# Performance work log

Hardware: AMD Instinct MI355X
Metric: run time of the kernel (lower is better)

Reference implementation:

```python
import jax, jax.numpy as jnp
import numpy as np

B, S, D, H = 2, 2048, 1024, 16
DK = D // H


def setup_inputs() -> dict:
    key = jax.random.key(0)
    ks = jax.random.split(key, 10)
    scale = 1.0 / np.sqrt(D)
    x = jax.random.normal(ks[0], (B, S, D), dtype=jnp.float32)
    # causal mask: 1 = attend, 0 = masked (module's create_causal_mask)
    mask = jnp.tril(jnp.ones((S, S), dtype=jnp.int32))[None, None]
    Wq = jax.random.normal(ks[1], (D, D), jnp.float32) * scale
    bq = jax.random.normal(ks[2], (D,), jnp.float32) * 0.01
    Wk = jax.random.normal(ks[3], (D, D), jnp.float32) * scale
    bk = jax.random.normal(ks[4], (D,), jnp.float32) * 0.01
    Wv = jax.random.normal(ks[5], (D, D), jnp.float32) * scale
    bv = jax.random.normal(ks[6], (D,), jnp.float32) * 0.01
    Wo = jax.random.normal(ks[7], (D, D), jnp.float32) * scale
    bo = jax.random.normal(ks[8], (D,), jnp.float32) * 0.01
    return {"x": x, "mask": mask, "Wq": Wq, "bq": bq, "Wk": Wk, "bk": bk,
            "Wv": Wv, "bv": bv, "Wo": Wo, "bo": bo}


def reference(x, mask, Wq, bq, Wk, bk, Wv, bv, Wo, bo):
    b, s, _ = x.shape
    # projections; [B,S,D] -> [B,H,S,DK]
    def split_heads(t):
        return t.reshape(b, s, H, DK).transpose(0, 2, 1, 3)
    Q = split_heads(x @ Wq + bq)
    K = split_heads(x @ Wk + bk)
    V = split_heads(x @ Wv + bv)
    scores = jnp.einsum('bhqd,bhkd->bhqk', Q, K) / np.sqrt(DK)
    scores = jnp.where(mask == 0, jnp.float32(-1e9), scores)
    attn = jax.nn.softmax(scores, axis=-1)  # dropout p=0 -> identity
    ctx = jnp.einsum('bhqk,bhkd->bhqd', attn, V)
    ctx = ctx.transpose(0, 2, 1, 3).reshape(b, s, D)
    return ctx @ Wo + bo
```

## Files before the change

### kernel.cpp

```cpp
#include <hip/hip_runtime.h>
#include <hip/hip_bf16.h>


typedef _Float16 f16x8 __attribute__((ext_vector_type(8)));
typedef _Float16 f16x4 __attribute__((ext_vector_type(4)));
typedef _Float16 f16x2 __attribute__((ext_vector_type(2)));
typedef float f32x4 __attribute__((ext_vector_type(4)));

#define QSCALE 0.180336880111112f

__device__ __forceinline__ void async_copy16(const _Float16* gsrc,
                                             _Float16* ldst) {
  __builtin_amdgcn_global_load_lds(
      (const __attribute__((address_space(1))) void*)gsrc,
      (__attribute__((address_space(3))) void*)ldst, 16, 0, 0);
}

__global__ __launch_bounds__(256) void prep(
    const float* __restrict__ x, _Float16* __restrict__ xh,
    const float* __restrict__ W0, const float* __restrict__ W1,
    const float* __restrict__ W2, const float* __restrict__ W3,
    _Float16* __restrict__ T0, _Float16* __restrict__ T1,
    _Float16* __restrict__ T2, _Float16* __restrict__ T3) {
  if (blockIdx.x < 4096) {
    int i = (blockIdx.x * 256 + threadIdx.x) * 4;
    float4 v = *(const float4*)(x + i);
    f16x4 o;
    o.x = (_Float16)v.x; o.y = (_Float16)v.y;
    o.z = (_Float16)v.z; o.w = (_Float16)v.w;
    *(f16x4*)(xh + i) = o;
    return;
  }
  const int id = blockIdx.x - 4096;
  const int w = id >> 10, rem = id & 1023;
  const int bx = rem & 31, by = rem >> 5;
  const float* W; _Float16* T;
  switch (w) {
    case 0: W = W0; T = T0; break;
    case 1: W = W1; T = T1; break;
    case 2: W = W2; T = T2; break;
    default: W = W3; T = T3; break;
  }
  __shared__ _Float16 tile[32][33];
  const int tx = threadIdx.x & 31, ty = threadIdx.x >> 5;
  const int n0 = bx * 32, k0 = by * 32;
  for (int i = 0; i < 4; i++) {
    int kk = k0 + ty + i * 8;
    tile[ty + i * 8][tx] = (_Float16)W[(size_t)kk * 1024 + n0 + tx];
  }
  __syncthreads();
  for (int i = 0; i < 4; i++) {
    int nn = n0 + ty + i * 8;
    T[(size_t)nn * 1024 + k0 + tx] = tile[tx][ty + i * 8];
  }
}

__global__ __launch_bounds__(256) void gemm_qkv(
    const _Float16* __restrict__ A, const _Float16* __restrict__ BtAll,
    const float* __restrict__ bq, const float* __restrict__ bk,
    const float* __restrict__ bv, _Float16* __restrict__ Qh,
    _Float16* __restrict__ Kh, _Float16* __restrict__ VT) {
  __shared__ _Float16 As[128 * 32];
  __shared__ _Float16 Bs[128 * 32];
  const int tid = threadIdx.x;
  const int wave = tid >> 6, lane = tid & 63;
  const int lr = lane & 15, lq = lane >> 4;
  const int m0 = blockIdx.x * 128, n0 = blockIdx.y * 128;
  const int rw = (wave & 1) * 64, cw = (wave >> 1) * 64;

  const int sel = blockIdx.y >> 3;
  const float* bias = sel == 0 ? bq : (sel == 1 ? bk : bv);
  const int c0 = n0 & 1023;

  f32x4 acc[4][4] = {};
  const int r0 = wave * 32 + (lane >> 2);
  const int woff = (lane & 3) * 8;

  for (int kt = 0; kt < 1024; kt += 32) {
    __syncthreads();
    async_copy16(A + (size_t)(m0 + r0) * 1024 + kt + woff, As + r0 * 32 + woff);
    async_copy16(A + (size_t)(m0 + r0 + 16) * 1024 + kt + woff,
                 As + (r0 + 16) * 32 + woff);
    async_copy16(BtAll + (size_t)(n0 + r0) * 1024 + kt + woff,
                 Bs + r0 * 32 + woff);
    async_copy16(BtAll + (size_t)(n0 + r0 + 16) * 1024 + kt + woff,
                 Bs + (r0 + 16) * 32 + woff);
    __syncthreads();
    f16x8 af[4], bf[4];
    for (int i = 0; i < 4; i++)
      af[i] = *(const f16x8*)(As + (rw + i * 16 + lr) * 32 + lq * 8);
    for (int j = 0; j < 4; j++)
      bf[j] = *(const f16x8*)(Bs + (cw + j * 16 + lr) * 32 + lq * 8);
    for (int i = 0; i < 4; i++)
      for (int j = 0; j < 4; j++)
        acc[i][j] = __builtin_amdgcn_mfma_f32_16x16x32_f16(af[i], bf[j],
                                                           acc[i][j], 0, 0, 0);
  }

  if (sel == 2) {
    for (int i = 0; i < 4; i++) {
      const int row = m0 + rw + i * 16 + lq * 4;
      const int bb = row >> 11, ss = row & 2047;
      for (int j = 0; j < 4; j++) {
        const int col = c0 + cw + j * 16 + lr;
        const int hh = col >> 6, dk = col & 63;
        const float bvl = bias[col];
        f16x4 pv;
        for (int r = 0; r < 4; r++) pv[r] = (_Float16)(acc[i][j][r] + bvl);
        *(f16x4*)(VT + ((size_t)(bb * 16 + hh) * 64 + dk) * 2048 + ss) = pv;
      }
    }
  } else {
    _Float16* out = sel == 0 ? Qh : Kh;
    const float scl = sel == 0 ? QSCALE : 1.0f;
    for (int i = 0; i < 4; i++) {
      const int row = m0 + rw + i * 16 + lq * 4;
      for (int j = 0; j < 4; j++) {
        const int col = c0 + cw + j * 16 + lr;
        const float bvl = bias[col];
        for (int r = 0; r < 4; r++)
          out[(size_t)(row + r) * 1024 + col] =
              (_Float16)((acc[i][j][r] + bvl) * scl);
      }
    }
  }
}

__global__ __launch_bounds__(256) void gemm_out(
    const _Float16* __restrict__ A, const _Float16* __restrict__ Bt,
    const float* __restrict__ bias, float* __restrict__ out) {
  __shared__ _Float16 As[128 * 32];
  __shared__ _Float16 Bs[64 * 32];
  const int tid = threadIdx.x;
  const int wave = tid >> 6, lane = tid & 63;
  const int lr = lane & 15, lq = lane >> 4;
  const int m0 = blockIdx.x * 128, n0 = blockIdx.y * 64;
  const int rw = (wave & 1) * 64, cw = (wave >> 1) * 32;
  f32x4 acc[4][2] = {};
  const int r0 = wave * 32 + (lane >> 2);
  const int br = tid >> 2;
  const int woff = (lane & 3) * 8;

  for (int kt = 0; kt < 1024; kt += 32) {
    __syncthreads();
    async_copy16(A + (size_t)(m0 + r0) * 1024 + kt + woff, As + r0 * 32 + woff);
    async_copy16(A + (size_t)(m0 + r0 + 16) * 1024 + kt + woff,
                 As + (r0 + 16) * 32 + woff);
    async_copy16(Bt + (size_t)(n0 + br) * 1024 + kt + woff,
                 Bs + br * 32 + woff);
    __syncthreads();
    f16x8 af[4], bf[2];
    for (int i = 0; i < 4; i++)
      af[i] = *(const f16x8*)(As + (rw + i * 16 + lr) * 32 + lq * 8);
    for (int j = 0; j < 2; j++)
      bf[j] = *(const f16x8*)(Bs + (cw + j * 16 + lr) * 32 + lq * 8);
    for (int i = 0; i < 4; i++)
      for (int j = 0; j < 2; j++)
        acc[i][j] = __builtin_amdgcn_mfma_f32_16x16x32_f16(af[i], bf[j],
                                                           acc[i][j], 0, 0, 0);
  }
  for (int i = 0; i < 4; i++) {
    const int row = m0 + rw + i * 16 + lq * 4;
    for (int j = 0; j < 2; j++) {
      const int col = n0 + cw + j * 16 + lr;
      const float bvl = bias[col];
      for (int r = 0; r < 4; r++)
        out[(size_t)(row + r) * 1024 + col] = acc[i][j][r] + bvl;
    }
  }
}

__global__ __launch_bounds__(256) void attn(const _Float16* __restrict__ Q,
                                            const _Float16* __restrict__ K,
                                            const _Float16* __restrict__ VT,
                                            _Float16* __restrict__ ctx) {
  const int qt = 15 - blockIdx.y;
  const int bh = blockIdx.x;
  const int b = bh >> 4, h = bh & 15;
  const int tid = threadIdx.x, wave = tid >> 6, lane = tid & 63;
  const int lr = lane & 15, lq = lane >> 4;
  const int qmin = qt * 128 + wave * 32;
  const size_t qkbase = ((size_t)b * 2048) * 1024 + h * 64;
  const size_t vtbase = ((size_t)bh) * 64 * 2048;

  __shared__ _Float16 Ks[2][64 * 72];
  __shared__ _Float16 Vs[2][64 * 72];

  f16x8 qf[2][2];
  for (int m = 0; m < 2; m++) {
    const _Float16* qp =
        Q + qkbase + (size_t)(qmin + m * 16 + lr) * 1024 + lq * 8;
    qf[m][0] = *(const f16x8*)qp;
    qf[m][1] = *(const f16x8*)(qp + 32);
  }

  float mrow[2] = {-1e30f, -1e30f}, lsum[2] = {0.f, 0.f};
  f32x4 o[2][4] = {};

  const int sgr = tid >> 2, sgc = (tid & 3) * 8;
  const _Float16* Kg0 = K + qkbase + (size_t)sgr * 1024 + sgc;
  const _Float16* Vg0 = VT + vtbase + (size_t)sgr * 2048 + sgc;
  uint4 ka = *(const uint4*)Kg0, kb = *(const uint4*)(Kg0 + 32);
  uint4 va = *(const uint4*)Vg0, vb = *(const uint4*)(Vg0 + 32);

  const int tmax = 2 * qt + 1;
  for (int t = 0;; t++) {
    _Float16* ksb = Ks[t & 1];
    _Float16* vsb = Vs[t & 1];
    *(uint4*)(ksb + sgr * 72 + sgc) = ka;
    *(uint4*)(ksb + sgr * 72 + sgc + 32) = kb;
    *(uint4*)(vsb + sgr * 72 + sgc) = va;
    *(uint4*)(vsb + sgr * 72 + sgc + 32) = vb;
    __syncthreads();
    if (t < tmax) {
      const _Float16* kg = Kg0 + (size_t)(t + 1) * 64 * 1024;
      const _Float16* vg = Vg0 + (t + 1) * 64;
      ka = *(const uint4*)kg; kb = *(const uint4*)(kg + 32);
      va = *(const uint4*)vg; vb = *(const uint4*)(vg + 32);
    }

    const int kv0 = t * 64;
    f32x4 s[2][4];
    for (int ks = 0; ks < 4; ks++) {
      f16x8 k0 = *(const f16x8*)(ksb + (ks * 16 + lr) * 72 + lq * 8);
      f16x8 k1 = *(const f16x8*)(ksb + (ks * 16 + lr) * 72 + 32 + lq * 8);
      for (int m = 0; m < 2; m++) {
        f32x4 z = {};
        z = __builtin_amdgcn_mfma_f32_16x16x32_f16(k0, qf[m][0], z, 0, 0, 0);
        z = __builtin_amdgcn_mfma_f32_16x16x32_f16(k1, qf[m][1], z, 0, 0, 0);
        s[m][ks] = z;
      }
    }
    if (kv0 + 63 > qmin) {
      for (int m = 0; m < 2; m++) {
        const int qcol = qmin + m * 16 + lr;
        for (int ks = 0; ks < 4; ks++)
          for (int r = 0; r < 4; r++)
            if (kv0 + ks * 16 + lq * 4 + r > qcol) s[m][ks][r] = -1e30f;
      }
    }
    f16x4 pa[2][4];
    float alpha[2];
    for (int m = 0; m < 2; m++) {
      float mx = s[m][0][0];
      for (int ks = 0; ks < 4; ks++)
        for (int r = 0; r < 4; r++) mx = fmaxf(mx, s[m][ks][r]);
      mx = fmaxf(mx, __shfl_xor(mx, 16));
      mx = fmaxf(mx, __shfl_xor(mx, 32));
      float mnew = fmaxf(mrow[m], mx);
      alpha[m] = exp2f(mrow[m] - mnew);
      mrow[m] = mnew;
      float rs = 0.f;
      for (int ks = 0; ks < 4; ks++) {
        float p0 = exp2f(s[m][ks][0] - mnew);
        float p1 = exp2f(s[m][ks][1] - mnew);
        float p2 = exp2f(s[m][ks][2] - mnew);
        float p3 = exp2f(s[m][ks][3] - mnew);
        rs += (p0 + p1) + (p2 + p3);
        f16x2 q01 =
            __builtin_bit_cast(f16x2, __builtin_amdgcn_cvt_pkrtz(p0, p1));
        f16x2 q23 =
            __builtin_bit_cast(f16x2, __builtin_amdgcn_cvt_pkrtz(p2, p3));
        pa[m][ks] = __builtin_shufflevector(q01, q23, 0, 1, 2, 3);
      }
      rs += __shfl_xor(rs, 16);
      rs += __shfl_xor(rs, 32);
      lsum[m] = lsum[m] * alpha[m] + rs;
    }
    if (__any((alpha[0] != 1.0f) | (alpha[1] != 1.0f))) {
      for (int m = 0; m < 2; m++) {
        float ar[4];
        for (int r = 0; r < 4; r++) ar[r] = __shfl(alpha[m], lq * 4 + r);
        for (int dn = 0; dn < 4; dn++)
          for (int r = 0; r < 4; r++) o[m][dn][r] *= ar[r];
      }
    }
    for (int ks = 0; ks < 4; ks++)
      for (int dn = 0; dn < 4; dn++) {
        f16x4 vf =
            *(const f16x4*)(vsb + (dn * 16 + lr) * 72 + ks * 16 + lq * 4);
        for (int m = 0; m < 2; m++)
          o[m][dn] = __builtin_amdgcn_mfma_f32_16x16x16f16(pa[m][ks], vf,
                                                           o[m][dn], 0, 0, 0);
      }
    if (t == tmax) break;
  }

  for (int m = 0; m < 2; m++) {
    for (int r = 0; r < 4; r++) {
      float lv = __shfl(lsum[m], lq * 4 + r);
      float inv = 1.0f / lv;
      const int row = qmin + m * 16 + lq * 4 + r;
      for (int dn = 0; dn < 4; dn++)
        ctx[qkbase + (size_t)row * 1024 + dn * 16 + lr] =
            (_Float16)(o[m][dn][r] * inv);
    }
  }
}

extern "C" void kernel_launch(void* const* d_in, const int* in_sizes, int n_in,
                              void* d_out, int out_size, void* d_ws,
                              size_t ws_size, hipStream_t stream) {
  const float* x  = (const float*)d_in[0];
  const float* Wq = (const float*)d_in[2];
  const float* bq = (const float*)d_in[3];
  const float* Wk = (const float*)d_in[4];
  const float* bk = (const float*)d_in[5];
  const float* Wv = (const float*)d_in[6];
  const float* bv = (const float*)d_in[7];
  const float* Wo = (const float*)d_in[8];
  const float* bo = (const float*)d_in[9];
  float* out = (float*)d_out;

  char* ws = (char*)d_ws;
  const size_t MB = 1 << 20;
  _Float16* xh  = (_Float16*)(ws);
  _Float16* WTs = (_Float16*)(ws + 8 * MB);
  _Float16* WqT = WTs;
  _Float16* WkT = (_Float16*)(ws + 10 * MB);
  _Float16* WvT = (_Float16*)(ws + 12 * MB);
  _Float16* WoT = (_Float16*)(ws + 14 * MB);
  _Float16* Qh  = (_Float16*)(ws + 16 * MB);
  _Float16* Kh  = (_Float16*)(ws + 24 * MB);
  _Float16* VT  = (_Float16*)(ws + 32 * MB);
  _Float16* ctx = (_Float16*)(ws);

  prep<<<8192, 256, 0, stream>>>(x, xh, Wq, Wk, Wv, Wo, WqT, WkT, WvT, WoT);
  gemm_qkv<<<dim3(32, 24), 256, 0, stream>>>(xh, WTs, bq, bk, bv, Qh, Kh, VT);
  attn<<<dim3(32, 16), 256, 0, stream>>>(Qh, Kh, VT, ctx);
  gemm_out<<<dim3(32, 16), 256, 0, stream>>>(ctx, WoT, bo, out);
}
```

Baseline: 215.4 us.

## Shrink attention tiles, balance causal work, MFMA row sums, coalesce V transpose

The attention kernel now uses 64-query blocks with 128 threads and a 32-row grid, with a snake-ordered query-tile mapping meant to even out causal work across blocks. The diagonal mask is applied only on the last tile. The softmax row sum is now computed with an extra MFMA against a ones vector instead of shuffle reductions, and a trailing barrier protects the double buffer. The V-transpose epilogue of the QKV GEMM is staged through shared memory so global stores become coalesced 16-byte writes, at the cost of extra LDS use and barriers.

```diff
diff --git a/kernel.cpp b/kernel.cpp
--- a/kernel.cpp
+++ b/kernel.cpp
@@ -62,6 +62,7 @@
     _Float16* __restrict__ Kh, _Float16* __restrict__ VT) {
   __shared__ _Float16 As[128 * 32];
   __shared__ _Float16 Bs[128 * 32];
+  __shared__ _Float16 tbuf[64 * 136];
   const int tid = threadIdx.x;
   const int wave = tid >> 6, lane = tid & 63;
   const int lr = lane & 15, lq = lane >> 4;
@@ -98,16 +99,29 @@
   }
 
   if (sel == 2) {
-    for (int i = 0; i < 4; i++) {
-      const int row = m0 + rw + i * 16 + lq * 4;
-      const int bb = row >> 11, ss = row & 2047;
-      for (int j = 0; j < 4; j++) {
-        const int col = c0 + cw + j * 16 + lr;
-        const int hh = col >> 6, dk = col & 63;
-        const float bvl = bias[col];
-        f16x4 pv;
-        for (int r = 0; r < 4; r++) pv[r] = (_Float16)(acc[i][j][r] + bvl);
-        *(f16x4*)(VT + ((size_t)(bb * 16 + hh) * 64 + dk) * 2048 + ss) = pv;
+    const int bb = m0 >> 11, ss0 = m0 & 2047;
+    const int cs = tid & 15, dkr = tid >> 4;
+    for (int jj = 0; jj < 2; jj++) {
+      __syncthreads();
+      if ((wave >> 1) == jj) {
+        for (int i = 0; i < 4; i++) {
+          const int sl = rw + i * 16 + lq * 4;
+          for (int j = 0; j < 4; j++) {
+            const int dk = j * 16 + lr;
+            const float bvl = bias[c0 + jj * 64 + dk];
+            f16x4 pv;
+            for (int r = 0; r < 4; r++) pv[r] = (_Float16)(acc[i][j][r] + bvl);
+            *(f16x4*)(tbuf + dk * 136 + sl) = pv;
+          }
+        }
+      }
+      __syncthreads();
+      const int hh = (c0 + jj * 64) >> 6;
+      _Float16* dst = VT + ((size_t)(bb * 16 + hh) * 64) * 2048 + ss0;
+      for (int k = 0; k < 4; k++) {
+        const int dk = dkr + k * 16;
+        *(uint4*)(dst + (size_t)dk * 2048 + cs * 8) =
+            *(const uint4*)(tbuf + dk * 136 + cs * 8);
       }
     }
   } else {
@@ -170,16 +184,23 @@
   }
 }
 
-__global__ __launch_bounds__(256) void attn(const _Float16* __restrict__ Q,
+__global__ __launch_bounds__(128) void attn(const _Float16* __restrict__ Q,
                                             const _Float16* __restrict__ K,
                                             const _Float16* __restrict__ VT,
                                             _Float16* __restrict__ ctx) {
-  const int qt = 15 - blockIdx.y;
+  const int qy = blockIdx.y, li = qy & 7;
+  int qt;
+  switch (qy >> 3) {
+    case 0: qt = 31 - li; break;
+    case 1: qt = 16 + li; break;
+    case 2: qt = 15 - li; break;
+    default: qt = li; break;
+  }
   const int bh = blockIdx.x;
   const int b = bh >> 4, h = bh & 15;
   const int tid = threadIdx.x, wave = tid >> 6, lane = tid & 63;
   const int lr = lane & 15, lq = lane >> 4;
-  const int qmin = qt * 128 + wave * 32;
+  const int qmin = qt * 64 + wave * 32;
   const size_t qkbase = ((size_t)b * 2048) * 1024 + h * 64;
   const size_t vtbase = ((size_t)bh) * 64 * 2048;
 
@@ -193,33 +214,42 @@
     qf[m][0] = *(const f16x8*)qp;
     qf[m][1] = *(const f16x8*)(qp + 32);
   }
-
-  float mrow[2] = {-1e30f, -1e30f}, lsum[2] = {0.f, 0.f};
+  f16x4 onesf;
+  {
+    _Float16 ov = (lr == 0) ? (_Float16)1.0f : (_Float16)0.0f;
+    for (int i = 0; i < 4; i++) onesf[i] = ov;
+  }
+
+  float mrow[2] = {-1e30f, -1e30f};
   f32x4 o[2][4] = {};
-
-  const int sgr = tid >> 2, sgc = (tid & 3) * 8;
+  f32x4 ol[2] = {};
+
+  const int sgr = tid >> 1, sgc = (tid & 1) * 32;
   const _Float16* Kg0 = K + qkbase + (size_t)sgr * 1024 + sgc;
   const _Float16* Vg0 = VT + vtbase + (size_t)sgr * 2048 + sgc;
-  uint4 ka = *(const uint4*)Kg0, kb = *(const uint4*)(Kg0 + 32);
-  uint4 va = *(const uint4*)Vg0, vb = *(const uint4*)(Vg0 + 32);
-
-  const int tmax = 2 * qt + 1;
-  for (int t = 0;; t++) {
+  uint4 kr[4], vr[4];
+  for (int c = 0; c < 4; c++) {
+    kr[c] = *(const uint4*)(Kg0 + c * 8);
+    vr[c] = *(const uint4*)(Vg0 + c * 8);
+  }
+
+  for (int t = 0; t <= qt; t++) {
     _Float16* ksb = Ks[t & 1];
     _Float16* vsb = Vs[t & 1];
-    *(uint4*)(ksb + sgr * 72 + sgc) = ka;
-    *(uint4*)(ksb + sgr * 72 + sgc + 32) = kb;
-    *(uint4*)(vsb + sgr * 72 + sgc) = va;
-    *(uint4*)(vsb + sgr * 72 + sgc + 32) = vb;
-    __syncthreads();
-    if (t < tmax) {
+    for (int c = 0; c < 4; c++) {
+      *(uint4*)(ksb + sgr * 72 + sgc + c * 8) = kr[c];
+      *(uint4*)(vsb + sgr * 72 + sgc + c * 8) = vr[c];
+    }
+    __syncthreads();
+    if (t < qt) {
       const _Float16* kg = Kg0 + (size_t)(t + 1) * 64 * 1024;
       const _Float16* vg = Vg0 + (t + 1) * 64;
-      ka = *(const uint4*)kg; kb = *(const uint4*)(kg + 32);
-      va = *(const uint4*)vg; vb = *(const uint4*)(vg + 32);
-    }
-
-    const int kv0 = t * 64;
+      for (int c = 0; c < 4; c++) {
+        kr[c] = *(const uint4*)(kg + c * 8);
+        vr[c] = *(const uint4*)(vg + c * 8);
+      }
+    }
+
     f32x4 s[2][4];
     for (int ks = 0; ks < 4; ks++) {
       f16x8 k0 = *(const f16x8*)(ksb + (ks * 16 + lr) * 72 + lq * 8);
@@ -231,7 +261,8 @@
         s[m][ks] = z;
       }
     }
-    if (kv0 + 63 > qmin) {
+    if (t == qt) {
+      const int kv0 = t * 64;
       for (int m = 0; m < 2; m++) {
         const int qcol = qmin + m * 16 + lr;
         for (int ks = 0; ks < 4; ks++)
@@ -250,22 +281,17 @@
       float mnew = fmaxf(mrow[m], mx);
       alpha[m] = exp2f(mrow[m] - mnew);
       mrow[m] = mnew;
-      float rs = 0.f;
       for (int ks = 0; ks < 4; ks++) {
         float p0 = exp2f(s[m][ks][0] - mnew);
         float p1 = exp2f(s[m][ks][1] - mnew);
         float p2 = exp2f(s[m][ks][2] - mnew);
         float p3 = exp2f(s[m][ks][3] - mnew);
-        rs += (p0 + p1) + (p2 + p3);
         f16x2 q01 =
             __builtin_bit_cast(f16x2, __builtin_amdgcn_cvt_pkrtz(p0, p1));
         f16x2 q23 =
             __builtin_bit_cast(f16x2, __builtin_amdgcn_cvt_pkrtz(p2, p3));
         pa[m][ks] = __builtin_shufflevector(q01, q23, 0, 1, 2, 3);
       }
-      rs += __shfl_xor(rs, 16);
-      rs += __shfl_xor(rs, 32);
-      lsum[m] = lsum[m] * alpha[m] + rs;
     }
     if (__any((alpha[0] != 1.0f) | (alpha[1] != 1.0f))) {
       for (int m = 0; m < 2; m++) {
@@ -273,6 +299,7 @@
         for (int r = 0; r < 4; r++) ar[r] = __shfl(alpha[m], lq * 4 + r);
         for (int dn = 0; dn < 4; dn++)
           for (int r = 0; r < 4; r++) o[m][dn][r] *= ar[r];
+        for (int r = 0; r < 4; r++) ol[m][r] *= ar[r];
       }
     }
     for (int ks = 0; ks < 4; ks++)
@@ -283,12 +310,16 @@
           o[m][dn] = __builtin_amdgcn_mfma_f32_16x16x16f16(pa[m][ks], vf,
                                                            o[m][dn], 0, 0, 0);
       }
-    if (t == tmax) break;
+    for (int ks = 0; ks < 4; ks++)
+      for (int m = 0; m < 2; m++)
+        ol[m] = __builtin_amdgcn_mfma_f32_16x16x16f16(pa[m][ks], onesf, ol[m],
+                                                      0, 0, 0);
+    __syncthreads();
   }
 
   for (int m = 0; m < 2; m++) {
     for (int r = 0; r < 4; r++) {
-      float lv = __shfl(lsum[m], lq * 4 + r);
+      float lv = __shfl(ol[m][r], lane & 48);
       float inv = 1.0f / lv;
       const int row = qmin + m * 16 + lq * 4 + r;
       for (int dn = 0; dn < 4; dn++)
@@ -327,6 +358,6 @@
 
   prep<<<8192, 256, 0, stream>>>(x, xh, Wq, Wk, Wv, Wo, WqT, WkT, WvT, WoT);
   gemm_qkv<<<dim3(32, 24), 256, 0, stream>>>(xh, WTs, bq, bk, bv, Qh, Kh, VT);
-  attn<<<dim3(32, 16), 256, 0, stream>>>(Qh, Kh, VT, ctx);
+  attn<<<dim3(32, 32), 128, 0, stream>>>(Qh, Kh, VT, ctx);
   gemm_out<<<dim3(32, 16), 256, 0, stream>>>(ctx, WoT, bo, out);
 }
```

New measurement: 252.2 us. 17.0% more time.
